# Kernel optimization log

Measured on AMD Instinct MI355X. Metric: run time of the kernel, lower is better.

## Reference

```python
import jax, jax.numpy as jnp
import numpy as np

M = 4096      # dictionary_size
D = 64        # feature dim
YD = 4        # output dim (y_dim)
FF = 0.999    # forgetting_factor
REG = 1e-2    # regularisation
JITTER = 1e-10
LS = 8.0      # RBF lengthscale


def rbf(a, b):
    # squared-distance RBF Gram via the ||a||^2 + ||b||^2 - 2ab^T identity
    a2 = jnp.sum(a * a, -1)[:, None]
    b2 = jnp.sum(b * b, -1)[None, :]
    d2 = jnp.maximum(a2 + b2 - 2.0 * (a @ b.T), 0.0)
    return jnp.exp(-d2 / (2.0 * LS * LS))


def setup_inputs() -> dict:
    key = jax.random.key(0)
    ks = jax.random.split(key, 7)
    return {
        'dictionary': jax.random.normal(ks[0], (M, D), jnp.float32),
        'mu': jax.random.normal(ks[1], (YD, M, 1), jnp.float32),
        'sigma': jax.random.normal(ks[2], (M, M), jnp.float32),
        'Q': jax.random.normal(ks[3], (M, M), jnp.float32),
        'x': jax.random.normal(ks[4], (D,), jnp.float32),
        'y': jax.random.normal(ks[5], (YD,), jnp.float32),
        'noise_num': jax.random.uniform(ks[6], (YD, 1, 1), jnp.float32),
        'noise_den': jnp.ones((1,), jnp.float32),
        'time_index': jnp.arange(M, dtype=jnp.float32),
        't': M,
    }


def reference(dictionary, mu, sigma, Q, x, y, noise_num, noise_den, time_index, t):
    alloc = time_index >= 0.0                      # (M,) bool: allocated slots
    y_ = y[:, None, None]                          # (YD,1,1)

    # --- B2P forgetting ---
    Kdd = rbf(dictionary, dictionary) * (alloc[:, None] * alloc[None, :])
    sig = FF * sigma + (1.0 - FF) * Kdd
    mu_f = jnp.sqrt(FF) * mu

    # --- kernel evals for new sample ---
    K_dx = rbf(dictionary, x[None, :]) * alloc[:, None]   # (M,1)
    K_xx = rbf(x[None, :], x[None, :]) + JITTER           # (1,1)

    q_ = Q @ K_dx                                         # (M,1)
    pu = jnp.maximum(K_xx - K_dx.T @ q_, 0.0)             # projection uncertainty (1,1)
    h_ = sig @ q_                                         # (M,1)
    npv = jnp.maximum(pu + q_.T @ h_, 0.0)                # noiseless predictive var (1,1)
    pred_mean = q_.T @ mu_f                               # (YD,1,1) via batched matmul
    pv = REG + npv

    # --- augmented (M+1) state ---
    p_ = jnp.concatenate((h_, npv), axis=-2)              # (M+1,1)
    mu_a = jnp.concatenate((mu_f, pred_mean), axis=-2) + (y_ - pred_mean) / pv * p_
    sig_a = jnp.block([[sig, h_], [h_.T, npv]]) - (p_ @ p_.T) / pv
    p2 = jnp.concatenate((q_, -jnp.ones((1, 1), q_.dtype)), axis=0)
    Q_a = jnp.pad(Q, ((0, 1), (0, 1))) + (p2 @ p2.T) / pu

    nnum = noise_num + FF * (y_ - pred_mean) ** 2 / pv
    nden = noise_den + FF

    # --- pruning criterion ---
    x_alloc = jnp.concatenate((alloc, jnp.ones((1,), bool)))

    def crit_low(_):
        return jnp.concatenate((jnp.ones((M, 1), Q_a.dtype), jnp.zeros((1, 1), Q_a.dtype)))

    def crit_mse(_):
        dq = jnp.where(~x_alloc, jnp.inf, jnp.diag(Q_a))
        errors = Q_a @ mu_a / dq[:, None]                 # (YD,M+1,1)
        return jnp.abs(errors).sum(-3)                    # (M+1,1)

    criterion = jax.lax.cond(pu.squeeze() < JITTER, crit_low, crit_mse, None)
    prune = jnp.argmin(criterion)
    denom = jnp.where(~x_alloc[prune], jnp.inf, Q_a[prune, prune])

    # swap (prune <-> last) permutation, then drop last row/col
    perm = jnp.arange(M + 1)
    perm = jnp.where(perm == prune, M, jnp.where(perm == M, prune, perm))

    Q_r = Q_a[perm, :]                                    # row swap
    Qs = Q_r[:-1, prune]                                  # column `prune` after row swap
    Q_n = Q_r[:, perm][:M, :M] - jnp.outer(Qs, Qs) / denom

    mu_n = mu_a[:, perm, :][:, :M, :]
    sig_n = sig_a[perm, :][:, perm][:M, :M]

    dict_n = dictionary.at[prune].set(x)
    ti_n = time_index.at[prune].set(jnp.asarray(t, time_index.dtype))
    alloc_n = ti_n >= 0.0
    sig_n = (alloc_n[:, None] * alloc_n[None, :]) * sig_n
    mu_n = jnp.where((ti_n < 0.0)[:, None], 0.0, mu_n)

    return (mu_n, sig_n, Q_n, dict_n, ti_n, nnum, nden)
```

## Files before the change

kernel.cpp:

```cpp
#include <hip/hip_runtime.h>
#include <math.h>

#define Mn 4096
#define Dn 64

#define OFF_A2   0
#define OFF_K    4096
#define OFF_Q    8192
#define OFF_H    12288
#define OFF_MUA  16384
#define OFF_QS   32772
#define OFF_QSD  36868
#define OFF_CRIT 40964
#define SC_PU    45064
#define SC_INVPU 45065
#define SC_NPV   45066
#define SC_PV    45067
#define SC_INVPV 45068
#define SC_DENOM 45069
#define SC_PRUNE 45070

#define O_MU   0
#define O_SIG  16384
#define O_Q    16793600
#define O_DICT 33570816
#define O_TI   33832960
#define O_NNUM 33837056
#define O_NDEN 33837060

__device__ __forceinline__ float waveReduceSum(float v) {
#pragma unroll
    for (int o = 32; o > 0; o >>= 1) v += __shfl_down(v, o);
    return v;
}

__global__ void k1_prep(const float* __restrict__ dict, const float* __restrict__ x,
                        const float* __restrict__ ti, float* __restrict__ ws) {
    int row  = blockIdx.x * 4 + (threadIdx.x >> 6);
    int lane = threadIdx.x & 63;
    float d  = dict[row * Dn + lane];
    float xv = x[lane];
    float a2 = waveReduceSum(d * d);
    float x2 = waveReduceSum(xv * xv);
    float dx = waveReduceSum(d * xv);
    if (lane == 0) {
        ws[OFF_A2 + row] = a2;
        float d2 = fmaxf(a2 + x2 - 2.0f * dx, 0.0f);
        float kv = expf(d2 * (-1.0f / 128.0f));
        ws[OFF_K + row] = (ti[row] >= 0.0f) ? kv : 0.0f;
    }
}

__global__ void k2_q(const float* __restrict__ Q, float* __restrict__ ws) {
    __shared__ float red[4];
    const int row = blockIdx.x;
    const int tid = threadIdx.x;
    const float* k  = ws + OFF_K;
    const float* Qr = Q + (size_t)row * Mn;
    float s = 0.0f;
    for (int j = tid; j < Mn; j += 256) s += Qr[j] * k[j];
    s = waveReduceSum(s);
    if ((tid & 63) == 0) red[tid >> 6] = s;
    __syncthreads();
    if (tid == 0) {
        ws[OFF_Q + row] = red[0] + red[1] + red[2] + red[3];
        ws[OFF_H + row] = 0.0f;
    }
}

__global__ __launch_bounds__(256) void k3_sig_h(
        const float* __restrict__ dict, const float* __restrict__ sigma,
        const float* __restrict__ ti, float* __restrict__ ws, float* __restrict__ out) {
    __shared__ float As[64 * 65];
    __shared__ float Bs[64 * 65];
    __shared__ float hred[64 * 16];
    const int tid = threadIdx.x;
    const int tx = tid & 15, ty = tid >> 4;
    const int r0 = blockIdx.y * 64;
    const int cchunk = blockIdx.x * 256;

    for (int l = 0; l < 16; ++l) {
        int lin = tid + l * 256;
        int row = lin >> 6, col = lin & 63;
        As[row * 65 + col] = dict[(size_t)(r0 + row) * Dn + col];
    }

    float a2i[4], ali[4];
#pragma unroll
    for (int r = 0; r < 4; ++r) {
        int gi = r0 + ty * 4 + r;
        a2i[r] = ws[OFF_A2 + gi];
        ali[r] = (ti[gi] >= 0.0f) ? 1.0f : 0.0f;
    }

    float hacc[4] = {0.f, 0.f, 0.f, 0.f};

    for (int ct = 0; ct < 4; ++ct) {
        const int c0 = cchunk + ct * 64;
        __syncthreads();
        for (int l = 0; l < 16; ++l) {
            int lin = tid + l * 256;
            int row = lin >> 6, col = lin & 63;
            Bs[row * 65 + col] = dict[(size_t)(c0 + row) * Dn + col];
        }
        __syncthreads();

        float acc[4][4];
#pragma unroll
        for (int r = 0; r < 4; ++r)
#pragma unroll
            for (int c = 0; c < 4; ++c) acc[r][c] = 0.0f;

#pragma unroll 8
        for (int kk = 0; kk < 64; ++kk) {
            float a[4], b[4];
#pragma unroll
            for (int r = 0; r < 4; ++r) a[r] = As[(ty * 4 + r) * 65 + kk];
#pragma unroll
            for (int c = 0; c < 4; ++c) b[c] = Bs[(tx * 4 + c) * 65 + kk];
#pragma unroll
            for (int r = 0; r < 4; ++r)
#pragma unroll
                for (int c = 0; c < 4; ++c) acc[r][c] = fmaf(a[r], b[c], acc[r][c]);
        }

        const int j = c0 + tx * 4;
        const float4 a2j4 = *(const float4*)(ws + OFF_A2 + j);
        const float4 qj4  = *(const float4*)(ws + OFF_Q + j);
        const float4 tj4  = *(const float4*)(ti + j);
        float a2j[4] = {a2j4.x, a2j4.y, a2j4.z, a2j4.w};
        float qj[4]  = {qj4.x, qj4.y, qj4.z, qj4.w};
        float alj[4] = {tj4.x >= 0.f ? 1.f : 0.f, tj4.y >= 0.f ? 1.f : 0.f,
                        tj4.z >= 0.f ? 1.f : 0.f, tj4.w >= 0.f ? 1.f : 0.f};

#pragma unroll
        for (int r = 0; r < 4; ++r) {
            const int gi = r0 + ty * 4 + r;
            const size_t off = (size_t)gi * Mn + j;
            const float4 sg = *(const float4*)(sigma + off);
            float sv[4] = {sg.x, sg.y, sg.z, sg.w};
            float res[4];
#pragma unroll
            for (int c = 0; c < 4; ++c) {
                float d2 = fmaxf(a2i[r] + a2j[c] - 2.0f * acc[r][c], 0.0f);
                float kv = __expf(d2 * (-1.0f / 128.0f)) * ali[r] * alj[c];
                res[c] = 0.999f * sv[c] + 0.001f * kv;
                hacc[r] += res[c] * qj[c];
            }
            float4 o = {res[0], res[1], res[2], res[3]};
            *(float4*)(out + O_SIG + off) = o;
        }
    }

    __syncthreads();
#pragma unroll
    for (int r = 0; r < 4; ++r) hred[(ty * 4 + r) * 16 + tx] = hacc[r];
    __syncthreads();
    if (tid < 64) {
        float s = 0.0f;
#pragma unroll
        for (int c = 0; c < 16; ++c) s += hred[tid * 16 + c];
        atomicAdd(ws + OFF_H + r0 + tid, s);
    }
}

__device__ __forceinline__ float blockReduce1024(float v, float* sred) {
    v = waveReduceSum(v);
    int tid = threadIdx.x;
    __syncthreads();
    if ((tid & 63) == 0) sred[tid >> 6] = v;
    __syncthreads();
    float r = 0.0f;
    if (tid == 0) {
#pragma unroll
        for (int i = 0; i < 16; ++i) r += sred[i];
    }
    return r;
}

__global__ __launch_bounds__(1024) void k4_scalars(
        const float* __restrict__ mu, const float* __restrict__ y,
        const float* __restrict__ nn, const float* __restrict__ nd,
        float* __restrict__ ws, float* __restrict__ out) {
    __shared__ float sred[16];
    __shared__ float sb[8];
    const int tid = threadIdx.x;
    const float* k = ws + OFF_K;
    const float* q = ws + OFF_Q;
    const float* h = ws + OFF_H;
    float kq = 0, qh = 0, p0 = 0, p1 = 0, p2 = 0, p3 = 0;
    for (int i = tid; i < Mn; i += 1024) {
        float qi = q[i];
        kq += k[i] * qi;
        qh += qi * h[i];
        p0 += qi * mu[0 * Mn + i];
        p1 += qi * mu[1 * Mn + i];
        p2 += qi * mu[2 * Mn + i];
        p3 += qi * mu[3 * Mn + i];
    }
    float rkq = blockReduce1024(kq, sred);
    float rqh = blockReduce1024(qh, sred);
    float r0 = blockReduce1024(p0, sred);
    float r1 = blockReduce1024(p1, sred);
    float r2 = blockReduce1024(p2, sred);
    float r3 = blockReduce1024(p3, sred);
    if (tid == 0) {
        const float sf = sqrtf(0.999f);
        float pu  = fmaxf(1.0f - rkq, 0.0f);
        float npv = fmaxf(pu + rqh, 0.0f);
        float pv  = 0.01f + npv;
        ws[SC_PU] = pu;
        ws[SC_INVPU] = 1.0f / pu;
        ws[SC_NPV] = npv;
        ws[SC_PV] = pv;
        ws[SC_INVPV] = 1.0f / pv;
        float pm[4] = {sf * r0, sf * r1, sf * r2, sf * r3};
#pragma unroll
        for (int yd = 0; yd < 4; ++yd) {
            float yv = y[yd];
            float dy = yv - pm[yd];
            float dl = dy / pv;
            sb[yd] = dl;
            ws[OFF_MUA + yd * (Mn + 1) + Mn] = pm[yd] + dl * npv;
            out[O_NNUM + yd] = nn[yd] + 0.999f * (dy * dy) / pv;
        }
        out[O_NDEN] = nd[0] + 0.999f;
    }
    __syncthreads();
    const float sf = sqrtf(0.999f);
    float d0 = sb[0], d1 = sb[1], d2 = sb[2], d3 = sb[3];
    for (int i = tid; i < Mn; i += 1024) {
        float hi = h[i];
        ws[OFF_MUA + 0 * (Mn + 1) + i] = sf * mu[0 * Mn + i] + d0 * hi;
        ws[OFF_MUA + 1 * (Mn + 1) + i] = sf * mu[1 * Mn + i] + d1 * hi;
        ws[OFF_MUA + 2 * (Mn + 1) + i] = sf * mu[2 * Mn + i] + d2 * hi;
        ws[OFF_MUA + 3 * (Mn + 1) + i] = sf * mu[3 * Mn + i] + d3 * hi;
    }
}

__global__ void k5_crit(const float* __restrict__ Q, const float* __restrict__ ti,
                        float* __restrict__ ws) {
    const int row  = blockIdx.x * 4 + (threadIdx.x >> 6);
    const int lane = threadIdx.x & 63;
    if (row > Mn) return;
    const float pu = ws[SC_PU];
    if (pu < 1e-10f) {
        if (lane == 0) ws[OFF_CRIT + row] = (row < Mn) ? 1.0f : 0.0f;
        return;
    }
    const float inv_pu = ws[SC_INVPU];
    const float* q = ws + OFF_Q;
    const float* mua = ws + OFF_MUA;
    const float p2i = (row < Mn) ? q[row] : -1.0f;
    const float* Qrow = Q + (size_t)row * Mn;
    float n0 = 0, n1 = 0, n2 = 0, n3 = 0;
    const bool rin = (row < Mn);
    for (int j = lane; j <= Mn; j += 64) {
        float p2j = (j < Mn) ? q[j] : -1.0f;
        float qa = p2i * p2j * inv_pu;
        if (rin && j < Mn) qa += Qrow[j];
        n0 += qa * mua[0 * (Mn + 1) + j];
        n1 += qa * mua[1 * (Mn + 1) + j];
        n2 += qa * mua[2 * (Mn + 1) + j];
        n3 += qa * mua[3 * (Mn + 1) + j];
    }
    n0 = waveReduceSum(n0);
    n1 = waveReduceSum(n1);
    n2 = waveReduceSum(n2);
    n3 = waveReduceSum(n3);
    if (lane == 0) {
        bool xa = (row == Mn) ? true : (ti[row] >= 0.0f);
        float crit = 0.0f;
        if (xa) {
            float dq = p2i * p2i * inv_pu + (rin ? Qrow[row] : 0.0f);
            crit = fabsf(n0 / dq) + fabsf(n1 / dq) + fabsf(n2 / dq) + fabsf(n3 / dq);
        }
        ws[OFF_CRIT + row] = crit;
    }
}

__global__ __launch_bounds__(1024) void k6_argmin(const float* __restrict__ Q,
                                                  const float* __restrict__ ti,
                                                  float* __restrict__ ws) {
    __shared__ float sval[1024];
    __shared__ int   sidx[1024];
    const int tid = threadIdx.x;
    float bv = INFINITY;
    int bi = Mn + 1;
    for (int i = tid; i <= Mn; i += 1024) {
        float v = ws[OFF_CRIT + i];
        if (v < bv) { bv = v; bi = i; }
    }
    sval[tid] = bv; sidx[tid] = bi;
    __syncthreads();
    for (int s = 512; s > 0; s >>= 1) {
        if (tid < s) {
            float ov = sval[tid + s]; int oi = sidx[tid + s];
            if (ov < sval[tid] || (ov == sval[tid] && oi < sidx[tid])) {
                sval[tid] = ov; sidx[tid] = oi;
            }
        }
        __syncthreads();
    }
    if (tid == 0) {
        int prune = sidx[0];
        ((int*)ws)[SC_PRUNE] = prune;
        float inv_pu = ws[SC_INVPU];
        bool xa = (prune == Mn) ? true : (ti[prune] >= 0.0f);
        float qap;
        if (prune < Mn) {
            float qp = ws[OFF_Q + prune];
            qap = Q[(size_t)prune * Mn + prune] + qp * qp * inv_pu;
        } else {
            qap = inv_pu;
        }
        ws[SC_DENOM] = xa ? qap : INFINITY;
    }
}

__global__ void k6b_vec(const float* __restrict__ Q, const float* __restrict__ dict,
                        const float* __restrict__ x, const float* __restrict__ ti,
                        const int* __restrict__ tptr, float* __restrict__ ws,
                        float* __restrict__ out) {
    const int tid = blockIdx.x * 256 + threadIdx.x;
    const int prune = ((const int*)ws)[SC_PRUNE];
    const int row = tid >> 6, col = tid & 63;
    out[O_DICT + tid] = (row == prune) ? x[col] : dict[tid];
    if (tid < Mn) {
        float tv = ti[tid];
        if (tid == prune) {
            int raw = *tptr;
            tv = (raw >= 0 && raw < (1 << 30)) ? (float)raw : __int_as_float(raw);
        }
        out[O_TI + tid] = tv;
        const float inv_pu = ws[SC_INVPU];
        const float denom  = ws[SC_DENOM];
        const float p2p = (prune < Mn) ? ws[OFF_Q + prune] : -1.0f;
        float qs;
        if (tid == prune) {
            qs = -p2p * inv_pu;
        } else {
            float base = (prune < Mn) ? Q[(size_t)tid * Mn + prune] : 0.0f;
            qs = base + ws[OFF_Q + tid] * p2p * inv_pu;
        }
        ws[OFF_QS + tid] = qs;
        ws[OFF_QSD + tid] = qs / denom;
    }
}

__global__ void k7_qn(const float* __restrict__ Q, float* __restrict__ out,
                      const float* __restrict__ ws) {
    const int i = blockIdx.x;
    const int prune = ((const int*)ws)[SC_PRUNE];
    const float inv_pu = ws[SC_INVPU];
    const float* q = ws + OFF_Q;
    const int pi = (i == prune) ? Mn : i;
    const bool piok = (pi < Mn);
    const float p2i = piok ? q[pi] : -1.0f;
    const float qsi = ws[OFF_QS + i];
    const float* Qrow = Q + (size_t)pi * Mn;
    float* orow = out + O_Q + (size_t)i * Mn;
    for (int j = threadIdx.x; j < Mn; j += 256) {
        float p2j = (j == prune) ? -1.0f : q[j];
        float base = (piok && j != prune) ? Qrow[j] : 0.0f;
        float qa = base + p2i * p2j * inv_pu;
        orow[j] = qa - qsi * ws[OFF_QSD + j];
    }
}

__global__ void k8_sign(float* __restrict__ out, const float* __restrict__ ws) {
    const int i = blockIdx.x;
    const int prune = ((const int*)ws)[SC_PRUNE];
    const float inv_pv = ws[SC_INVPV];
    const float npv = ws[SC_NPV];
    const float* h = ws + OFF_H;
    const bool ip = (i == prune);
    const float ai = (out[O_TI + i] >= 0.0f) ? 1.0f : 0.0f;
    const float p_i = ip ? npv : h[i];
    const float hi = h[i];
    float* srow = out + O_SIG + (size_t)i * Mn;
    for (int j = threadIdx.x; j < Mn; j += 256) {
        const bool jp = (j == prune);
        float p_j = jp ? npv : h[j];
        float base;
        if (!ip && !jp) base = srow[j];
        else if (ip && jp) base = npv;
        else if (ip) base = h[j];
        else base = hi;
        float aj = (out[O_TI + j] >= 0.0f) ? 1.0f : 0.0f;
        srow[j] = ai * aj * (base - p_i * p_j * inv_pv);
    }
}

__global__ void k9_mun(float* __restrict__ out, const float* __restrict__ ws) {
    const int idx = blockIdx.x * 256 + threadIdx.x;
    const int prune = ((const int*)ws)[SC_PRUNE];
    const int yd = idx >> 12;
    const int i  = idx & (Mn - 1);
    float tin = out[O_TI + i];
    float v;
    if (tin < 0.0f) v = 0.0f;
    else v = ws[OFF_MUA + yd * (Mn + 1) + ((i == prune) ? Mn : i)];
    out[O_MU + idx] = v;
}

extern "C" void kernel_launch(void* const* d_in, const int* in_sizes, int n_in,
                              void* d_out, int out_size, void* d_ws, size_t ws_size,
                              hipStream_t stream) {
    const float* dict  = (const float*)d_in[0];
    const float* mu    = (const float*)d_in[1];
    const float* sigma = (const float*)d_in[2];
    const float* Q     = (const float*)d_in[3];
    const float* x     = (const float*)d_in[4];
    const float* y     = (const float*)d_in[5];
    const float* nn    = (const float*)d_in[6];
    const float* nd    = (const float*)d_in[7];
    const float* ti    = (const float*)d_in[8];
    const int*   tptr  = (const int*)d_in[9];
    float* out = (float*)d_out;
    float* ws  = (float*)d_ws;

    k1_prep<<<1024, 256, 0, stream>>>(dict, x, ti, ws);
    k2_q<<<4096, 256, 0, stream>>>(Q, ws);
    k3_sig_h<<<dim3(16, 64), 256, 0, stream>>>(dict, sigma, ti, ws, out);
    k4_scalars<<<1, 1024, 0, stream>>>(mu, y, nn, nd, ws, out);
    k5_crit<<<1025, 256, 0, stream>>>(Q, ti, ws);
    k6_argmin<<<1, 1024, 0, stream>>>(Q, ti, ws);
    k6b_vec<<<1024, 256, 0, stream>>>(Q, dict, x, ti, tptr, ws, out);
    k7_qn<<<4096, 256, 0, stream>>>(Q, out, ws);
    k8_sign<<<4096, 256, 0, stream>>>(out, ws);
    k9_mun<<<64, 256, 0, stream>>>(out, ws);
}
```

Measured before the change: 414.0 us.

## Vectorize memory-bound kernels with float4 and transpose GEMM tiles in LDS

Converts the row-streaming kernels (Q·k matvec, criterion, Q update, sigma update) to float4 loads and stores. The criterion kernel now uses one 256-thread block per row instead of one wavefront per row. The mu_a stride is padded to 4104 so rows are 16-byte aligned, and the workspace offsets are repacked, with OFF_CRIT now sharing the A2 slot. The Gram tile in k3 is stored transposed in LDS so each kk step needs only two float4 LDS reads, and the loop is fully unrolled. The aim is higher effective bandwidth and fewer scalar memory instructions, at the cost of more register pressure and special-case handling of the prune column.

```diff
diff --git a/kernel.cpp b/kernel.cpp
--- a/kernel.cpp
+++ b/kernel.cpp
@@ -3,22 +3,23 @@
 
 #define Mn 4096
 #define Dn 64
+#define MUA_STRIDE 4104
 
 #define OFF_A2   0
+#define OFF_CRIT 0
 #define OFF_K    4096
 #define OFF_Q    8192
 #define OFF_H    12288
 #define OFF_MUA  16384
-#define OFF_QS   32772
-#define OFF_QSD  36868
-#define OFF_CRIT 40964
-#define SC_PU    45064
-#define SC_INVPU 45065
-#define SC_NPV   45066
-#define SC_PV    45067
-#define SC_INVPV 45068
-#define SC_DENOM 45069
-#define SC_PRUNE 45070
+#define OFF_QS   32800
+#define OFF_QSD  36896
+#define SC_PU    40992
+#define SC_INVPU 40993
+#define SC_NPV   40994
+#define SC_PV    40995
+#define SC_INVPV 40996
+#define SC_DENOM 40997
+#define SC_PRUNE 40998
 
 #define O_MU   0
 #define O_SIG  16384
@@ -55,10 +56,15 @@
     __shared__ float red[4];
     const int row = blockIdx.x;
     const int tid = threadIdx.x;
-    const float* k  = ws + OFF_K;
-    const float* Qr = Q + (size_t)row * Mn;
+    const float4* Qr = (const float4*)(Q + (size_t)row * Mn);
+    const float4* kv = (const float4*)(ws + OFF_K);
     float s = 0.0f;
-    for (int j = tid; j < Mn; j += 256) s += Qr[j] * k[j];
+#pragma unroll
+    for (int it = 0; it < 4; ++it) {
+        int u = tid + it * 256;
+        float4 a = Qr[u], b = kv[u];
+        s += a.x * b.x + a.y * b.y + a.z * b.z + a.w * b.w;
+    }
     s = waveReduceSum(s);
     if ((tid & 63) == 0) red[tid >> 6] = s;
     __syncthreads();
@@ -68,21 +74,28 @@
     }
 }
 
-__global__ __launch_bounds__(256) void k3_sig_h(
+__global__ __launch_bounds__(256, 4) void k3_sig_h(
         const float* __restrict__ dict, const float* __restrict__ sigma,
         const float* __restrict__ ti, float* __restrict__ ws, float* __restrict__ out) {
-    __shared__ float As[64 * 65];
-    __shared__ float Bs[64 * 65];
+    __shared__ __align__(16) float At[64 * 68];
+    __shared__ __align__(16) float Bt[64 * 68];
     __shared__ float hred[64 * 16];
     const int tid = threadIdx.x;
     const int tx = tid & 15, ty = tid >> 4;
     const int r0 = blockIdx.y * 64;
     const int cchunk = blockIdx.x * 256;
-
-    for (int l = 0; l < 16; ++l) {
-        int lin = tid + l * 256;
-        int row = lin >> 6, col = lin & 63;
-        As[row * 65 + col] = dict[(size_t)(r0 + row) * Dn + col];
+    const int pidx = ((tid & 15) << 4) | (tid >> 4);
+
+#pragma unroll
+    for (int l = 0; l < 4; ++l) {
+        int u = pidx + l * 256;
+        int row = u >> 4;
+        int col = (u & 15) << 2;
+        float4 v = *(const float4*)(dict + (size_t)(r0 + row) * Dn + col);
+        At[(col + 0) * 68 + row] = v.x;
+        At[(col + 1) * 68 + row] = v.y;
+        At[(col + 2) * 68 + row] = v.z;
+        At[(col + 3) * 68 + row] = v.w;
     }
 
     float a2i[4], ali[4];
@@ -98,10 +111,16 @@
     for (int ct = 0; ct < 4; ++ct) {
         const int c0 = cchunk + ct * 64;
         __syncthreads();
-        for (int l = 0; l < 16; ++l) {
-            int lin = tid + l * 256;
-            int row = lin >> 6, col = lin & 63;
-            Bs[row * 65 + col] = dict[(size_t)(c0 + row) * Dn + col];
+#pragma unroll
+        for (int l = 0; l < 4; ++l) {
+            int u = pidx + l * 256;
+            int row = u >> 4;
+            int col = (u & 15) << 2;
+            float4 v = *(const float4*)(dict + (size_t)(c0 + row) * Dn + col);
+            Bt[(col + 0) * 68 + row] = v.x;
+            Bt[(col + 1) * 68 + row] = v.y;
+            Bt[(col + 2) * 68 + row] = v.z;
+            Bt[(col + 3) * 68 + row] = v.w;
         }
         __syncthreads();
 
@@ -111,17 +130,26 @@
 #pragma unroll
             for (int c = 0; c < 4; ++c) acc[r][c] = 0.0f;
 
-#pragma unroll 8
+#pragma unroll
         for (int kk = 0; kk < 64; ++kk) {
-            float a[4], b[4];
-#pragma unroll
-            for (int r = 0; r < 4; ++r) a[r] = As[(ty * 4 + r) * 65 + kk];
-#pragma unroll
-            for (int c = 0; c < 4; ++c) b[c] = Bs[(tx * 4 + c) * 65 + kk];
-#pragma unroll
-            for (int r = 0; r < 4; ++r)
-#pragma unroll
-                for (int c = 0; c < 4; ++c) acc[r][c] = fmaf(a[r], b[c], acc[r][c]);
+            float4 av = *(const float4*)(At + kk * 68 + (ty << 2));
+            float4 bv = *(const float4*)(Bt + kk * 68 + (tx << 2));
+            acc[0][0] = fmaf(av.x, bv.x, acc[0][0]);
+            acc[0][1] = fmaf(av.x, bv.y, acc[0][1]);
+            acc[0][2] = fmaf(av.x, bv.z, acc[0][2]);
+            acc[0][3] = fmaf(av.x, bv.w, acc[0][3]);
+            acc[1][0] = fmaf(av.y, bv.x, acc[1][0]);
+            acc[1][1] = fmaf(av.y, bv.y, acc[1][1]);
+            acc[1][2] = fmaf(av.y, bv.z, acc[1][2]);
+            acc[1][3] = fmaf(av.y, bv.w, acc[1][3]);
+            acc[2][0] = fmaf(av.z, bv.x, acc[2][0]);
+            acc[2][1] = fmaf(av.z, bv.y, acc[2][1]);
+            acc[2][2] = fmaf(av.z, bv.z, acc[2][2]);
+            acc[2][3] = fmaf(av.z, bv.w, acc[2][3]);
+            acc[3][0] = fmaf(av.w, bv.x, acc[3][0]);
+            acc[3][1] = fmaf(av.w, bv.y, acc[3][1]);
+            acc[3][2] = fmaf(av.w, bv.z, acc[3][2]);
+            acc[3][3] = fmaf(av.w, bv.w, acc[3][3]);
         }
 
         const int j = c0 + tx * 4;
@@ -221,7 +249,7 @@
             float dy = yv - pm[yd];
             float dl = dy / pv;
             sb[yd] = dl;
-            ws[OFF_MUA + yd * (Mn + 1) + Mn] = pm[yd] + dl * npv;
+            ws[OFF_MUA + yd * MUA_STRIDE + Mn] = pm[yd] + dl * npv;
             out[O_NNUM + yd] = nn[yd] + 0.999f * (dy * dy) / pv;
         }
         out[O_NDEN] = nd[0] + 0.999f;
@@ -231,49 +259,75 @@
     float d0 = sb[0], d1 = sb[1], d2 = sb[2], d3 = sb[3];
     for (int i = tid; i < Mn; i += 1024) {
         float hi = h[i];
-        ws[OFF_MUA + 0 * (Mn + 1) + i] = sf * mu[0 * Mn + i] + d0 * hi;
-        ws[OFF_MUA + 1 * (Mn + 1) + i] = sf * mu[1 * Mn + i] + d1 * hi;
-        ws[OFF_MUA + 2 * (Mn + 1) + i] = sf * mu[2 * Mn + i] + d2 * hi;
-        ws[OFF_MUA + 3 * (Mn + 1) + i] = sf * mu[3 * Mn + i] + d3 * hi;
-    }
-}
-
-__global__ void k5_crit(const float* __restrict__ Q, const float* __restrict__ ti,
-                        float* __restrict__ ws) {
-    const int row  = blockIdx.x * 4 + (threadIdx.x >> 6);
-    const int lane = threadIdx.x & 63;
-    if (row > Mn) return;
+        ws[OFF_MUA + 0 * MUA_STRIDE + i] = sf * mu[0 * Mn + i] + d0 * hi;
+        ws[OFF_MUA + 1 * MUA_STRIDE + i] = sf * mu[1 * Mn + i] + d1 * hi;
+        ws[OFF_MUA + 2 * MUA_STRIDE + i] = sf * mu[2 * Mn + i] + d2 * hi;
+        ws[OFF_MUA + 3 * MUA_STRIDE + i] = sf * mu[3 * Mn + i] + d3 * hi;
+    }
+}
+
+__global__ __launch_bounds__(256) void k5_crit(const float* __restrict__ Q,
+                                               const float* __restrict__ ti,
+                                               float* __restrict__ ws) {
+    __shared__ float sred[4][4];
+    const int row = blockIdx.x;
+    const int tid = threadIdx.x;
     const float pu = ws[SC_PU];
     if (pu < 1e-10f) {
-        if (lane == 0) ws[OFF_CRIT + row] = (row < Mn) ? 1.0f : 0.0f;
+        if (tid == 0) ws[OFF_CRIT + row] = (row < Mn) ? 1.0f : 0.0f;
         return;
     }
     const float inv_pu = ws[SC_INVPU];
-    const float* q = ws + OFF_Q;
+    const bool rin = (row < Mn);
+    const float p2i = rin ? ws[OFF_Q + row] : -1.0f;
+    const float4* q4  = (const float4*)(ws + OFF_Q);
+    const float4* Qr4 = (const float4*)(Q + (size_t)row * Mn);
     const float* mua = ws + OFF_MUA;
-    const float p2i = (row < Mn) ? q[row] : -1.0f;
-    const float* Qrow = Q + (size_t)row * Mn;
     float n0 = 0, n1 = 0, n2 = 0, n3 = 0;
-    const bool rin = (row < Mn);
-    for (int j = lane; j <= Mn; j += 64) {
-        float p2j = (j < Mn) ? q[j] : -1.0f;
-        float qa = p2i * p2j * inv_pu;
-        if (rin && j < Mn) qa += Qrow[j];
-        n0 += qa * mua[0 * (Mn + 1) + j];
-        n1 += qa * mua[1 * (Mn + 1) + j];
-        n2 += qa * mua[2 * (Mn + 1) + j];
-        n3 += qa * mua[3 * (Mn + 1) + j];
+#pragma unroll
+    for (int it = 0; it < 4; ++it) {
+        int u = tid + it * 256;
+        float4 qv = q4[u];
+        float4 base = rin ? Qr4[u] : make_float4(0.f, 0.f, 0.f, 0.f);
+        float4 qa;
+        qa.x = base.x + p2i * qv.x * inv_pu;
+        qa.y = base.y + p2i * qv.y * inv_pu;
+        qa.z = base.z + p2i * qv.z * inv_pu;
+        qa.w = base.w + p2i * qv.w * inv_pu;
+        const float4 m0 = *(const float4*)(mua + 0 * MUA_STRIDE + u * 4);
+        const float4 m1 = *(const float4*)(mua + 1 * MUA_STRIDE + u * 4);
+        const float4 m2 = *(const float4*)(mua + 2 * MUA_STRIDE + u * 4);
+        const float4 m3 = *(const float4*)(mua + 3 * MUA_STRIDE + u * 4);
+        n0 += qa.x * m0.x + qa.y * m0.y + qa.z * m0.z + qa.w * m0.w;
+        n1 += qa.x * m1.x + qa.y * m1.y + qa.z * m1.z + qa.w * m1.w;
+        n2 += qa.x * m2.x + qa.y * m2.y + qa.z * m2.z + qa.w * m2.w;
+        n3 += qa.x * m3.x + qa.y * m3.y + qa.z * m3.z + qa.w * m3.w;
     }
     n0 = waveReduceSum(n0);
     n1 = waveReduceSum(n1);
     n2 = waveReduceSum(n2);
     n3 = waveReduceSum(n3);
-    if (lane == 0) {
-        bool xa = (row == Mn) ? true : (ti[row] >= 0.0f);
+    if ((tid & 63) == 0) {
+        int w = tid >> 6;
+        sred[w][0] = n0; sred[w][1] = n1; sred[w][2] = n2; sred[w][3] = n3;
+    }
+    __syncthreads();
+    if (tid == 0) {
+        float t0 = 0, t1 = 0, t2 = 0, t3 = 0;
+#pragma unroll
+        for (int w = 0; w < 4; ++w) {
+            t0 += sred[w][0]; t1 += sred[w][1]; t2 += sred[w][2]; t3 += sred[w][3];
+        }
+        float qaM = -p2i * inv_pu;
+        t0 += qaM * mua[0 * MUA_STRIDE + Mn];
+        t1 += qaM * mua[1 * MUA_STRIDE + Mn];
+        t2 += qaM * mua[2 * MUA_STRIDE + Mn];
+        t3 += qaM * mua[3 * MUA_STRIDE + Mn];
+        bool xa = rin ? (ti[row] >= 0.0f) : true;
         float crit = 0.0f;
         if (xa) {
-            float dq = p2i * p2i * inv_pu + (rin ? Qrow[row] : 0.0f);
-            crit = fabsf(n0 / dq) + fabsf(n1 / dq) + fabsf(n2 / dq) + fabsf(n3 / dq);
+            float dq = rin ? (Q[(size_t)row * Mn + row] + p2i * p2i * inv_pu) : inv_pu;
+            crit = fabsf(t0 / dq) + fabsf(t1 / dq) + fabsf(t2 / dq) + fabsf(t3 / dq);
         }
         ws[OFF_CRIT + row] = crit;
     }
@@ -351,44 +405,73 @@
 __global__ void k7_qn(const float* __restrict__ Q, float* __restrict__ out,
                       const float* __restrict__ ws) {
     const int i = blockIdx.x;
+    const int tid = threadIdx.x;
     const int prune = ((const int*)ws)[SC_PRUNE];
     const float inv_pu = ws[SC_INVPU];
-    const float* q = ws + OFF_Q;
     const int pi = (i == prune) ? Mn : i;
     const bool piok = (pi < Mn);
-    const float p2i = piok ? q[pi] : -1.0f;
+    const float p2i = piok ? ws[OFF_Q + pi] : -1.0f;
     const float qsi = ws[OFF_QS + i];
-    const float* Qrow = Q + (size_t)pi * Mn;
-    float* orow = out + O_Q + (size_t)i * Mn;
-    for (int j = threadIdx.x; j < Mn; j += 256) {
-        float p2j = (j == prune) ? -1.0f : q[j];
-        float base = (piok && j != prune) ? Qrow[j] : 0.0f;
-        float qa = base + p2i * p2j * inv_pu;
-        orow[j] = qa - qsi * ws[OFF_QSD + j];
+    const float4* Qr4  = (const float4*)(Q + (size_t)pi * Mn);
+    const float4* q4   = (const float4*)(ws + OFF_Q);
+    const float4* qsd4 = (const float4*)(ws + OFF_QSD);
+    float4* o4 = (float4*)(out + O_Q + (size_t)i * Mn);
+#pragma unroll
+    for (int it = 0; it < 4; ++it) {
+        int u = tid + it * 256;
+        float4 base = piok ? Qr4[u] : make_float4(0.f, 0.f, 0.f, 0.f);
+        float4 p2j = q4[u];
+        if ((prune >> 2) == u) {
+            int c = prune & 3;
+            ((float*)&p2j)[c] = -1.0f;
+            ((float*)&base)[c] = 0.0f;
+        }
+        float4 d = qsd4[u];
+        float4 r;
+        r.x = base.x + p2i * p2j.x * inv_pu - qsi * d.x;
+        r.y = base.y + p2i * p2j.y * inv_pu - qsi * d.y;
+        r.z = base.z + p2i * p2j.z * inv_pu - qsi * d.z;
+        r.w = base.w + p2i * p2j.w * inv_pu - qsi * d.w;
+        o4[u] = r;
     }
 }
 
 __global__ void k8_sign(float* __restrict__ out, const float* __restrict__ ws) {
     const int i = blockIdx.x;
+    const int tid = threadIdx.x;
     const int prune = ((const int*)ws)[SC_PRUNE];
     const float inv_pv = ws[SC_INVPV];
     const float npv = ws[SC_NPV];
-    const float* h = ws + OFF_H;
     const bool ip = (i == prune);
     const float ai = (out[O_TI + i] >= 0.0f) ? 1.0f : 0.0f;
-    const float p_i = ip ? npv : h[i];
-    const float hi = h[i];
-    float* srow = out + O_SIG + (size_t)i * Mn;
-    for (int j = threadIdx.x; j < Mn; j += 256) {
-        const bool jp = (j == prune);
-        float p_j = jp ? npv : h[j];
-        float base;
-        if (!ip && !jp) base = srow[j];
-        else if (ip && jp) base = npv;
-        else if (ip) base = h[j];
-        else base = hi;
-        float aj = (out[O_TI + j] >= 0.0f) ? 1.0f : 0.0f;
-        srow[j] = ai * aj * (base - p_i * p_j * inv_pv);
+    const float hi = ws[OFF_H + i];
+    const float p_i = ip ? npv : hi;
+    const float4* h4  = (const float4*)(ws + OFF_H);
+    const float4* ti4 = (const float4*)(out + O_TI);
+    float4* s4 = (float4*)(out + O_SIG + (size_t)i * Mn);
+#pragma unroll
+    for (int it = 0; it < 4; ++it) {
+        int u = tid + it * 256;
+        float4 sv = s4[u];
+        float4 hj = h4[u];
+        float4 tv = ti4[u];
+        float pj[4] = {hj.x, hj.y, hj.z, hj.w};
+        float bs[4];
+        if (ip) { bs[0] = hj.x; bs[1] = hj.y; bs[2] = hj.z; bs[3] = hj.w; }
+        else    { bs[0] = sv.x; bs[1] = sv.y; bs[2] = sv.z; bs[3] = sv.w; }
+        if ((prune >> 2) == u) {
+            int c = prune & 3;
+            pj[c] = npv;
+            bs[c] = ip ? npv : hi;
+        }
+        float aj[4] = {tv.x >= 0.f ? 1.f : 0.f, tv.y >= 0.f ? 1.f : 0.f,
+                       tv.z >= 0.f ? 1.f : 0.f, tv.w >= 0.f ? 1.f : 0.f};
+        float4 r;
+        r.x = ai * aj[0] * (bs[0] - p_i * pj[0] * inv_pv);
+        r.y = ai * aj[1] * (bs[1] - p_i * pj[1] * inv_pv);
+        r.z = ai * aj[2] * (bs[2] - p_i * pj[2] * inv_pv);
+        r.w = ai * aj[3] * (bs[3] - p_i * pj[3] * inv_pv);
+        s4[u] = r;
     }
 }
 
@@ -400,7 +483,7 @@
     float tin = out[O_TI + i];
     float v;
     if (tin < 0.0f) v = 0.0f;
-    else v = ws[OFF_MUA + yd * (Mn + 1) + ((i == prune) ? Mn : i)];
+    else v = ws[OFF_MUA + yd * MUA_STRIDE + ((i == prune) ? Mn : i)];
     out[O_MU + idx] = v;
 }
 
@@ -424,7 +507,7 @@
     k2_q<<<4096, 256, 0, stream>>>(Q, ws);
     k3_sig_h<<<dim3(16, 64), 256, 0, stream>>>(dict, sigma, ti, ws, out);
     k4_scalars<<<1, 1024, 0, stream>>>(mu, y, nn, nd, ws, out);
-    k5_crit<<<1025, 256, 0, stream>>>(Q, ti, ws);
+    k5_crit<<<4097, 256, 0, stream>>>(Q, ti, ws);
     k6_argmin<<<1, 1024, 0, stream>>>(Q, ti, ws);
     k6b_vec<<<1024, 256, 0, stream>>>(Q, dict, x, ti, tptr, ws, out);
     k7_qn<<<4096, 256, 0, stream>>>(Q, out, ws);
```

Result: faster. 345.2 us (-16.6%).
